# Kernel optimization log

Hardware: AMD Instinct MI355X
Metric: run time of the kernel (lower is better)

Reference implementation:

```python
import jax, jax.numpy as jnp
import numpy as np

DIM = 256
HEADS = 8
M = 16                      # window_size
Mo = int((1 + 0.5) * M)     # overlapped window = 24
TABLE = (M + Mo - 2) * (2 * Mo) + 1  # 1825
B = 256                     # batch * num_windows


def _relative_position_index():
    ch = np.arange(M)
    cw = np.arange(Mo)
    gh = np.stack(np.meshgrid(ch, ch, indexing='ij')).reshape(2, -1)   # (2, M^2)
    gw = np.stack(np.meshgrid(cw, cw, indexing='ij')).reshape(2, -1)   # (2, Mo^2)
    rel = gh[:, :, None] - gw[:, None, :]          # (2, M^2, Mo^2)
    rel = rel.transpose(1, 2, 0)
    rel[:, :, 0] += Mo - 1
    rel[:, :, 1] += Mo - 1
    rel[:, :, 0] *= 2 * Mo - 1
    return rel.sum(-1).astype(np.int32)            # (M^2, Mo^2)


def setup_inputs() -> dict:
    key = jax.random.key(0)
    ks = jax.random.split(key, 9)
    inp = {
        'q_w': jax.random.normal(ks[0], (B, M * M, DIM), jnp.float32),
        'kv_w': jax.random.normal(ks[1], (B, Mo * Mo, DIM), jnp.float32),
        'q_W': jax.random.normal(ks[2], (DIM, DIM), jnp.float32) * 0.02,
        'q_b': jnp.zeros((DIM,), jnp.float32),
        'kv_W': jax.random.normal(ks[3], (DIM, 2 * DIM), jnp.float32) * 0.02,
        'kv_b': jnp.zeros((2 * DIM,), jnp.float32),
        'proj_W': jax.random.normal(ks[4], (DIM, DIM), jnp.float32) * 0.02,
        'proj_b': jnp.zeros((DIM,), jnp.float32),
        'bias_table': jax.random.normal(ks[5], (TABLE, HEADS), jnp.float32) * 0.02,
        'rel_index': jnp.asarray(_relative_position_index()),
    }
    return inp


def reference(q_w, kv_w, q_W, q_b, kv_W, kv_b, proj_W, proj_b, bias_table, rel_index):
    Dh = DIM // HEADS
    scale = Dh ** (-0.5)
    Nq, Nk = M * M, Mo * Mo
    # q projection -> (B, H, Nq, Dh)
    q = (q_w @ q_W + q_b).reshape(B, Nq, HEADS, Dh).transpose(0, 2, 1, 3)
    # kv projection -> k, v each (B, H, Nk, Dh)
    kv = (kv_w @ kv_W + kv_b).reshape(B, Nk, 2, HEADS, Dh)
    k = kv[:, :, 0].transpose(0, 2, 1, 3)
    v = kv[:, :, 1].transpose(0, 2, 1, 3)
    # scaled scores + gathered relative-position bias
    attn = jnp.einsum('bhqd,bhkd->bhqk', q * scale, k)
    bias = bias_table[rel_index.reshape(-1)].reshape(Nq, Nk, HEADS)
    attn = attn + bias.transpose(2, 0, 1)[None]     # (B, H, Nq, Nk)
    attn = jax.nn.softmax(attn, axis=-1)
    out = jnp.einsum('bhqk,bhkd->bhqd', attn, v)
    out = out.transpose(0, 2, 1, 3).reshape(B, Nq, DIM)
    return out @ proj_W + proj_b
```

## Files before the change

### kernel.cpp

```cpp
#include <hip/hip_runtime.h>
#include <hip/hip_bf16.h>

typedef __hip_bfloat16 bf16;
typedef __attribute__((ext_vector_type(8))) short bf16x8;
typedef __attribute__((ext_vector_type(4))) float floatx4;
typedef __attribute__((ext_vector_type(4))) unsigned short u16x4;

#define L2E 1.4426950408889634f
#define SCALE_L2E (0.17677669529663687f * 1.4426950408889634f)
#define MFMA16 __builtin_amdgcn_mfma_f32_16x16x32_bf16

__device__ __forceinline__ short f2bs(float x) {
  union { bf16 h; short s; } u; u.h = __float2bfloat16(x); return u.s;
}
__device__ __forceinline__ float ldf(const void* p, size_t i, bool f32) {
  return f32 ? ((const float*)p)[i] : __bfloat162float(((const bf16*)p)[i]);
}
__device__ __forceinline__ float bs2f(unsigned short u) {
  union { unsigned short u; bf16 h; } v; v.u = u; return __bfloat162float(v.h);
}
__device__ __forceinline__ unsigned int pkbf(float a, float b) {
  union { bf16 h; unsigned short s; } ua, ub;
  ua.h = __float2bfloat16(a); ub.h = __float2bfloat16(b);
  return (unsigned int)ua.s | ((unsigned int)ub.s << 16);
}
__device__ __forceinline__ bf16x8 load8(const void* p, size_t idx, bool f32) {
  if (f32) {
    const floatx4* fp = (const floatx4*)((const float*)p + idx);
    floatx4 a = fp[0], b = fp[1];
    bf16x8 r;
    r[0] = f2bs(a[0]); r[1] = f2bs(a[1]); r[2] = f2bs(a[2]); r[3] = f2bs(a[3]);
    r[4] = f2bs(b[0]); r[5] = f2bs(b[1]); r[6] = f2bs(b[2]); r[7] = f2bs(b[3]);
    return r;
  }
  return *(const bf16x8*)((const bf16*)p + idx);
}
__device__ __forceinline__ int xcd_remap(int bid, int nwg) {
  int q = nwg >> 3, r = nwg & 7, x = bid & 7, loc = bid >> 3;
  int base = (x < r) ? x * (q + 1) : r * (q + 1) + (x - r) * q;
  return base + loc;
}

__global__ void detect_dtype(const unsigned short* __restrict__ q_w_u16, int* __restrict__ flag) {
  int tid = threadIdx.x;
  int cnt = 0;
  for (int i = tid; i < 4096; i += 64) {
    int e = (q_w_u16[i] >> 7) & 0xFF;
    cnt += (e >= 145);
  }
  #pragma unroll
  for (int off = 32; off; off >>= 1) cnt += __shfl_down(cnt, off);
  if (tid == 0) *flag = (cnt >= 16) ? 1 : 0;
}

__global__ __launch_bounds__(256) void transpose_w(const void* __restrict__ src,
                                                   bf16* __restrict__ dst, int N,
                                                   const int* __restrict__ flagp) {
  __shared__ bf16 t[32][33];
  const bool f = (*flagp != 0);
  int bx = blockIdx.x * 32;
  int by = blockIdx.y * 32;
  int x = threadIdx.x & 31, y = threadIdx.x >> 5;
  #pragma unroll
  for (int yy = y; yy < 32; yy += 8)
    t[yy][x] = __float2bfloat16(ldf(src, (size_t)(by + yy) * N + bx + x, f));
  __syncthreads();
  #pragma unroll
  for (int yy = y; yy < 32; yy += 8)
    dst[(size_t)(bx + yy) * 256 + by + x] = t[x][yy];
}

__global__ __launch_bounds__(256) void bias_expand(const void* __restrict__ table,
                                                   const int* __restrict__ relidx,
                                                   bf16* __restrict__ biasFb,
                                                   const int* __restrict__ flagp) {
  const bool f = (*flagp != 0);
  int i = blockIdx.x * 256 + threadIdx.x;
  int q = i / 576, k = i - q * 576;
  int idx = relidx[i];
  size_t off = ((size_t)(q >> 4) * 36 + (k >> 4)) * 256 + (q & 15) * 16 + (k & 15);
  #pragma unroll
  for (int h = 0; h < 8; h++)
    biasFb[(size_t)h * 147456 + off] =
        __float2bfloat16(ldf(table, (size_t)idx * 8 + h, f) * L2E);
}

template <int EPI>
__global__ __launch_bounds__(256) void gemm_bt(const void* __restrict__ A, size_t a_off,
                                               const bf16* __restrict__ BT,
                                               const void* __restrict__ bias,
                                               void* __restrict__ C, size_t c_off,
                                               bf16* __restrict__ C2,
                                               const int* __restrict__ flagp) {
  __shared__ __align__(16) bf16 As[128 * 40];
  __shared__ __align__(16) bf16 Bs[128 * 40];
  const bool f = (*flagp != 0);
  const bool af = (EPI == 0) ? false : f;
  const int tid = threadIdx.x;
  const int wave = tid >> 6, lane = tid & 63;
  const int q4 = lane >> 4, l16 = lane & 15;
  constexpr int NT = (EPI == 2) ? 4 : 2;
  constexpr int LNT = (EPI == 2) ? 2 : 1;
  const int L = xcd_remap(blockIdx.x, gridDim.x);
  const int m0 = (L >> LNT) * 128, n0 = (L & (NT - 1)) * 128;
  const int wm = (wave & 1) * 64, wn = (wave >> 1) * 64;
  const int sr = tid >> 2, sc = (tid & 3) * 8;
  floatx4 acc[4][4];
  #pragma unroll
  for (int i = 0; i < 4; i++)
    #pragma unroll
    for (int j = 0; j < 4; j++) acc[i][j] = (floatx4){0.f, 0.f, 0.f, 0.f};

  const size_t abase = a_off + (size_t)(m0 + sr) * 256 + sc;
  const bf16* Bp = BT + (size_t)(n0 + sr) * 256 + sc;
  for (int k0 = 0; k0 < 256; k0 += 32) {
    *(bf16x8*)&As[sr * 40 + sc]        = load8(A, abase + k0, af);
    *(bf16x8*)&As[(sr + 64) * 40 + sc] = load8(A, abase + 64 * 256 + k0, af);
    *(bf16x8*)&Bs[sr * 40 + sc]        = *(const bf16x8*)(Bp + k0);
    *(bf16x8*)&Bs[(sr + 64) * 40 + sc] = *(const bf16x8*)(Bp + 64 * 256 + k0);
    __syncthreads();
    bf16x8 afr[4], bfr[4];
    #pragma unroll
    for (int i = 0; i < 4; i++)
      afr[i] = *(const bf16x8*)&As[(wm + i * 16 + l16) * 40 + q4 * 8];
    #pragma unroll
    for (int j = 0; j < 4; j++)
      bfr[j] = *(const bf16x8*)&Bs[(wn + j * 16 + l16) * 40 + q4 * 8];
    #pragma unroll
    for (int i = 0; i < 4; i++)
      #pragma unroll
      for (int j = 0; j < 4; j++)
        acc[i][j] = MFMA16(afr[i], bfr[j], acc[i][j], 0, 0, 0);
    __syncthreads();
  }
  #pragma unroll
  for (int i = 0; i < 4; i++) {
    #pragma unroll
    for (int j = 0; j < 4; j++) {
      int mrow = m0 + wm + i * 16 + q4 * 4;
      int ncol = n0 + wn + j * 16 + l16;
      float bv = ldf(bias, ncol, f);
      #pragma unroll
      for (int r = 0; r < 4; r++) {
        float v = acc[i][j][r] + bv;
        int m_e = mrow + r;
        if (EPI == 0) {
          size_t oi = c_off + (size_t)m_e * 256 + ncol;
          if (f) ((float*)C)[oi] = v;
          else   ((bf16*)C)[oi] = __float2bfloat16(v);
        } else if (EPI == 1) {
          ((bf16*)C)[(size_t)m_e * 256 + ncol] = __float2bfloat16(v * SCALE_L2E);
        } else {
          int bb = m_e / 576;
          int nn = m_e - bb * 576;
          if (ncol < 256) {
            int hh = ncol >> 5, dd = ncol & 31;
            ((bf16*)C)[(((size_t)bb * 8 + hh) * 576 + nn) * 32 + dd] = __float2bfloat16(v);
          } else {
            int cc = ncol - 256;
            int hh = cc >> 5, dd = cc & 31;
            int kt = nn >> 6, kvl = nn & 63;
            C2[((((size_t)bb * 8 + hh) * 9 + kt) * 32 + dd) * 64 + kvl] = __float2bfloat16(v);
          }
        }
      }
    }
  }
}

__global__ __launch_bounds__(256, 4) void attn(const bf16* __restrict__ Q,
                                               const bf16* __restrict__ Kc,
                                               const bf16* __restrict__ Vc,
                                               const bf16* __restrict__ biasF,
                                               bf16* __restrict__ O,
                                               int nwg) {
  __shared__ __align__(16) bf16 Ks[2][64][32];
  __shared__ __align__(16) bf16 Vs[2][32][64];
  __shared__ __align__(16) bf16 P[4][16][72];
  __shared__ float SCb[4][16];
  const int tid = threadIdx.x, wave = tid >> 6, lane = tid & 63;
  const int q4 = lane >> 4, l16 = lane & 15;
  const int L = xcd_remap(blockIdx.x, nwg);
  const int b = L >> 5, h = (L >> 2) & 7, qc = L & 3;
  const int q0 = qc * 64 + wave * 16;
  const int qb = qc * 4 + wave;

  bf16x8 qf = *(const bf16x8*)&Q[((size_t)b * 256 + q0 + l16) * 256 + h * 32 + q4 * 8];
  const bf16* kg = Kc + ((size_t)b * 8 + h) * 18432;
  const bf16* vg = Vc + ((size_t)b * 8 + h) * 18432;
  const unsigned short* bp =
      (const unsigned short*)biasF + ((size_t)h * 16 + qb) * 9216 + l16 * 16 + q4 * 4;

  bf16* ksd = &Ks[0][tid >> 2][(((tid & 3) ^ ((tid >> 2) & 3))) * 8];
  bf16* vsd = &Vs[0][tid >> 3][(((tid & 7) ^ ((tid >> 3) & 7))) * 8];
  const int kx = (l16 & 3);
  const int vx = (l16 & 7);

  float m = 0.f, l = 0.f;
  floatx4 o0 = (floatx4){0.f, 0.f, 0.f, 0.f};
  floatx4 o1 = (floatx4){0.f, 0.f, 0.f, 0.f};

  {
    bf16x8 k0r = *(const bf16x8*)(kg + tid * 8);
    bf16x8 v0r = *(const bf16x8*)(vg + tid * 8);
    *(bf16x8*)ksd = k0r;
    *(bf16x8*)vsd = v0r;
  }
  u16x4 bfr[4];
  #pragma unroll
  for (int t = 0; t < 4; t++) bfr[t] = *(const u16x4*)(bp + t * 256);
  asm volatile("s_waitcnt lgkmcnt(0)" ::: "memory");
  __builtin_amdgcn_sched_barrier(0);
  __builtin_amdgcn_s_barrier();
  __builtin_amdgcn_sched_barrier(0);

  #pragma unroll 1
  for (int it = 0; it < 9; it++) {
    const int cur = it & 1;
    const int nx = (cur ^ 1) * 2048;
    bf16x8 kNr, vNr; u16x4 bn[4];
    if (it < 8) {
      kNr = *(const bf16x8*)(kg + (it + 1) * 2048 + tid * 8);
      vNr = *(const bf16x8*)(vg + (it + 1) * 2048 + tid * 8);
      #pragma unroll
      for (int t = 0; t < 4; t++) bn[t] = *(const u16x4*)(bp + (it + 1) * 1024 + t * 256);
    }
    floatx4 s[4];
    __builtin_amdgcn_s_setprio(1);
    #pragma unroll
    for (int t = 0; t < 4; t++) {
      bf16x8 kf = *(const bf16x8*)&Ks[cur][t * 16 + l16][(q4 ^ kx) * 8];
      floatx4 c;
      #pragma unroll
      for (int r = 0; r < 4; r++) c[r] = bs2f(bfr[t][r]);
      s[t] = MFMA16(kf, qf, c, 0, 0, 0);
    }
    __builtin_amdgcn_s_setprio(0);
    float tm = fmaxf(fmaxf(fmaxf(s[0][0], s[0][1]), fmaxf(s[0][2], s[0][3])),
                     fmaxf(fmaxf(s[1][0], s[1][1]), fmaxf(s[1][2], s[1][3])));
    tm = fmaxf(tm, fmaxf(fmaxf(fmaxf(s[2][0], s[2][1]), fmaxf(s[2][2], s[2][3])),
                         fmaxf(fmaxf(s[3][0], s[3][1]), fmaxf(s[3][2], s[3][3]))));
    tm = fmaxf(tm, __shfl_xor(tm, 16));
    tm = fmaxf(tm, __shfl_xor(tm, 32));
    float p[4][4];
    #pragma unroll
    for (int t = 0; t < 4; t++)
      #pragma unroll
      for (int r = 0; r < 4; r++)
        p[t][r] = __builtin_amdgcn_exp2f(s[t][r] - m);
    float rs = ((p[0][0] + p[0][1]) + (p[0][2] + p[0][3])) +
               ((p[1][0] + p[1][1]) + (p[1][2] + p[1][3])) +
               ((p[2][0] + p[2][1]) + (p[2][2] + p[2][3])) +
               ((p[3][0] + p[3][1]) + (p[3][2] + p[3][3]));
    if (__any(tm > m + 8.f)) {
      float mn = fmaxf(m, tm);
      float sc = __builtin_amdgcn_exp2f(m - mn);
      #pragma unroll
      for (int t = 0; t < 4; t++)
        #pragma unroll
        for (int r = 0; r < 4; r++) p[t][r] *= sc;
      rs *= sc;
      l *= sc;
      if (q4 == 0) SCb[wave][l16] = sc;
      floatx4 sv = *(const floatx4*)&SCb[wave][q4 * 4];
      #pragma unroll
      for (int r = 0; r < 4; r++) { o0[r] *= sv[r]; o1[r] *= sv[r]; }
      m = mn;
    }
    rs += __shfl_xor(rs, 16);
    rs += __shfl_xor(rs, 32);
    l += rs;
    #pragma unroll
    for (int t = 0; t < 4; t++) {
      uint2 w;
      w.x = pkbf(p[t][0], p[t][1]);
      w.y = pkbf(p[t][2], p[t][3]);
      *(uint2*)&P[wave][l16][t * 16 + q4 * 4] = w;
    }
    bf16x8 pf0 = *(const bf16x8*)&P[wave][l16][q4 * 8];
    bf16x8 pf1 = *(const bf16x8*)&P[wave][l16][32 + q4 * 8];
    bf16x8 v00 = *(const bf16x8*)&Vs[cur][l16][((q4 ^ vx)) * 8];
    bf16x8 v01 = *(const bf16x8*)&Vs[cur][l16 + 16][((q4 ^ vx)) * 8];
    bf16x8 v10 = *(const bf16x8*)&Vs[cur][l16][(((4 + q4) ^ vx)) * 8];
    bf16x8 v11 = *(const bf16x8*)&Vs[cur][l16 + 16][(((4 + q4) ^ vx)) * 8];
    __builtin_amdgcn_s_setprio(1);
    o0 = MFMA16(pf0, v00, o0, 0, 0, 0);
    o1 = MFMA16(pf0, v01, o1, 0, 0, 0);
    o0 = MFMA16(pf1, v10, o0, 0, 0, 0);
    o1 = MFMA16(pf1, v11, o1, 0, 0, 0);
    __builtin_amdgcn_s_setprio(0);
    if (it < 8) {
      *(bf16x8*)(ksd + nx) = kNr;
      *(bf16x8*)(vsd + nx) = vNr;
      #pragma unroll
      for (int t = 0; t < 4; t++) bfr[t] = bn[t];
    }
    asm volatile("s_waitcnt lgkmcnt(0)" ::: "memory");
    __builtin_amdgcn_sched_barrier(0);
    __builtin_amdgcn_s_barrier();
    __builtin_amdgcn_sched_barrier(0);
  }
  float invl = 1.f / l;
  if (q4 == 0) SCb[wave][l16] = invl;
  floatx4 iv = *(const floatx4*)&SCb[wave][q4 * 4];
  bf16* op = O + ((size_t)b * 256 + q0 + q4 * 4) * 256 + h * 32;
  #pragma unroll
  for (int r = 0; r < 4; r++) {
    op[(size_t)r * 256 + l16]      = __float2bfloat16(o0[r] * iv[r]);
    op[(size_t)r * 256 + 16 + l16] = __float2bfloat16(o1[r] * iv[r]);
  }
}

extern "C" void kernel_launch(void* const* d_in, const int* in_sizes, int n_in,
                              void* d_out, int out_size, void* d_ws, size_t ws_size,
                              hipStream_t stream) {
  const void* q_w    = d_in[0];
  const void* kv_w   = d_in[1];
  const void* q_Wm   = d_in[2];
  const void* q_b    = d_in[3];
  const void* kv_Wm  = d_in[4];
  const void* kv_b   = d_in[5];
  const void* proj_Wm= d_in[6];
  const void* proj_b = d_in[7];
  const void* btab   = d_in[8];
  const int*  relidx = (const int*)d_in[9];

  const size_t FIXED = 256 + 131072 + 262144 + 131072 + 2359296;
  int W = 2;
  {
    const int cand[8] = {256, 128, 64, 32, 16, 8, 4, 2};
    for (int i = 0; i < 8; i++) {
      if (ws_size >= FIXED + (size_t)cand[i] * 851968ULL) { W = cand[i]; break; }
    }
  }
  const int NCH = 256 / W;

  char* ws = (char*)d_ws;
  int*  flag  = (int*)(ws);
  bf16* WqT   = (bf16*)(ws + 256);
  bf16* WkvT  = (bf16*)(ws + 131328);
  bf16* WpT   = (bf16*)(ws + 393472);
  bf16* biasFb= (bf16*)(ws + 524544);
  char* cb    = ws + FIXED;
  const size_t qsz = (size_t)W * 131072ULL;
  const size_t ksz = (size_t)W * 294912ULL;
  bf16* Qs   = (bf16*)(cb);
  bf16* Kb   = (bf16*)(cb + qsz);
  bf16* Vt   = (bf16*)(cb + qsz + ksz);
  bf16* Obuf = (bf16*)(cb + qsz + 2 * ksz);

  detect_dtype<<<1, 64, 0, stream>>>((const unsigned short*)q_w, flag);
  transpose_w<<<dim3(8, 8),  256, 0, stream>>>(q_Wm,   WqT,  256, flag);
  transpose_w<<<dim3(16, 8), 256, 0, stream>>>(kv_Wm,  WkvT, 512, flag);
  transpose_w<<<dim3(8, 8),  256, 0, stream>>>(proj_Wm,WpT,  256, flag);
  bias_expand<<<576, 256, 0, stream>>>(btab, relidx, biasFb, flag);

  for (int c = 0; c < NCH; c++) {
    const size_t qoff = (size_t)c * W * 65536;
    const size_t koff = (size_t)c * W * 147456;
    gemm_bt<1><<<4 * W, 256, 0, stream>>>(q_w, qoff, WqT, q_b, Qs, 0, nullptr, flag);
    gemm_bt<2><<<18 * W, 256, 0, stream>>>(kv_w, koff, WkvT, kv_b, Kb, 0, Vt, flag);
    attn<<<W * 32, 256, 0, stream>>>(Qs, Kb, Vt, biasFb, Obuf, W * 32);
    gemm_bt<0><<<4 * W, 256, 0, stream>>>(Obuf, 0, WpT, proj_b, d_out, qoff, nullptr, flag);
  }
}
```

Before: 638.2 us.

## Double-buffer GEMM shared tiles with register prefetch and vectorize V-transpose stores

The projection GEMM now uses two LDS buffers. Global loads for the next K-slice are issued into registers before the MFMA work on the current slice, and the fp32-to-bf16 conversion is split out so it happens after the math. This removes one barrier per iteration and hides global latency. The V-transposed epilogue also writes four contiguous bf16 values as one 8-byte store instead of four scalar stores, relying on 4-row groups never crossing a 576 batch boundary or a 64 tile. The cost is doubled LDS use and more live registers, which may reduce occupancy.

```diff
diff --git a/kernel.cpp b/kernel.cpp
--- a/kernel.cpp
+++ b/kernel.cpp
@@ -24,16 +24,26 @@
   ua.h = __float2bfloat16(a); ub.h = __float2bfloat16(b);
   return (unsigned int)ua.s | ((unsigned int)ub.s << 16);
 }
-__device__ __forceinline__ bf16x8 load8(const void* p, size_t idx, bool f32) {
+struct APre { floatx4 x, y; };
+__device__ __forceinline__ APre loadA(const void* p, size_t idx, bool f32) {
+  APre r;
   if (f32) {
     const floatx4* fp = (const floatx4*)((const float*)p + idx);
-    floatx4 a = fp[0], b = fp[1];
+    r.x = fp[0]; r.y = fp[1];
+  } else {
+    r.x = *(const floatx4*)((const bf16*)p + idx);
+    r.y = r.x;
+  }
+  return r;
+}
+__device__ __forceinline__ bf16x8 cvtA(const APre& a, bool f32) {
+  if (f32) {
     bf16x8 r;
-    r[0] = f2bs(a[0]); r[1] = f2bs(a[1]); r[2] = f2bs(a[2]); r[3] = f2bs(a[3]);
-    r[4] = f2bs(b[0]); r[5] = f2bs(b[1]); r[6] = f2bs(b[2]); r[7] = f2bs(b[3]);
+    r[0] = f2bs(a.x[0]); r[1] = f2bs(a.x[1]); r[2] = f2bs(a.x[2]); r[3] = f2bs(a.x[3]);
+    r[4] = f2bs(a.y[0]); r[5] = f2bs(a.y[1]); r[6] = f2bs(a.y[2]); r[7] = f2bs(a.y[3]);
     return r;
   }
-  return *(const bf16x8*)((const bf16*)p + idx);
+  union { floatx4 f; bf16x8 h; } u; u.f = a.x; return u.h;
 }
 __device__ __forceinline__ int xcd_remap(int bid, int nwg) {
   int q = nwg >> 3, r = nwg & 7, x = bid & 7, loc = bid >> 3;
@@ -92,8 +102,8 @@
                                                void* __restrict__ C, size_t c_off,
                                                bf16* __restrict__ C2,
                                                const int* __restrict__ flagp) {
-  __shared__ __align__(16) bf16 As[128 * 40];
-  __shared__ __align__(16) bf16 Bs[128 * 40];
+  __shared__ __align__(16) bf16 As[2][128 * 40];
+  __shared__ __align__(16) bf16 Bs[2][128 * 40];
   const bool f = (*flagp != 0);
   const bool af = (EPI == 0) ? false : f;
   const int tid = threadIdx.x;
@@ -113,26 +123,50 @@
 
   const size_t abase = a_off + (size_t)(m0 + sr) * 256 + sc;
   const bf16* Bp = BT + (size_t)(n0 + sr) * 256 + sc;
-  for (int k0 = 0; k0 < 256; k0 += 32) {
-    *(bf16x8*)&As[sr * 40 + sc]        = load8(A, abase + k0, af);
-    *(bf16x8*)&As[(sr + 64) * 40 + sc] = load8(A, abase + 64 * 256 + k0, af);
-    *(bf16x8*)&Bs[sr * 40 + sc]        = *(const bf16x8*)(Bp + k0);
-    *(bf16x8*)&Bs[(sr + 64) * 40 + sc] = *(const bf16x8*)(Bp + 64 * 256 + k0);
-    __syncthreads();
+
+  {
+    APre a0 = loadA(A, abase, af);
+    APre a1 = loadA(A, abase + 64 * 256, af);
+    bf16x8 b0 = *(const bf16x8*)(Bp);
+    bf16x8 b1 = *(const bf16x8*)(Bp + 64 * 256);
+    *(bf16x8*)&As[0][sr * 40 + sc]        = cvtA(a0, af);
+    *(bf16x8*)&As[0][(sr + 64) * 40 + sc] = cvtA(a1, af);
+    *(bf16x8*)&Bs[0][sr * 40 + sc]        = b0;
+    *(bf16x8*)&Bs[0][(sr + 64) * 40 + sc] = b1;
+  }
+  __syncthreads();
+
+  #pragma unroll
+  for (int t = 0; t < 8; t++) {
+    const int cur = t & 1, nxt = cur ^ 1;
+    APre na0, na1; bf16x8 nb0, nb1;
+    if (t < 7) {
+      na0 = loadA(A, abase + (t + 1) * 32, af);
+      na1 = loadA(A, abase + 64 * 256 + (t + 1) * 32, af);
+      nb0 = *(const bf16x8*)(Bp + (t + 1) * 32);
+      nb1 = *(const bf16x8*)(Bp + 64 * 256 + (t + 1) * 32);
+    }
     bf16x8 afr[4], bfr[4];
     #pragma unroll
     for (int i = 0; i < 4; i++)
-      afr[i] = *(const bf16x8*)&As[(wm + i * 16 + l16) * 40 + q4 * 8];
+      afr[i] = *(const bf16x8*)&As[cur][(wm + i * 16 + l16) * 40 + q4 * 8];
     #pragma unroll
     for (int j = 0; j < 4; j++)
-      bfr[j] = *(const bf16x8*)&Bs[(wn + j * 16 + l16) * 40 + q4 * 8];
+      bfr[j] = *(const bf16x8*)&Bs[cur][(wn + j * 16 + l16) * 40 + q4 * 8];
     #pragma unroll
     for (int i = 0; i < 4; i++)
       #pragma unroll
       for (int j = 0; j < 4; j++)
         acc[i][j] = MFMA16(afr[i], bfr[j], acc[i][j], 0, 0, 0);
-    __syncthreads();
-  }
+    if (t < 7) {
+      *(bf16x8*)&As[nxt][sr * 40 + sc]        = cvtA(na0, af);
+      *(bf16x8*)&As[nxt][(sr + 64) * 40 + sc] = cvtA(na1, af);
+      *(bf16x8*)&Bs[nxt][sr * 40 + sc]        = nb0;
+      *(bf16x8*)&Bs[nxt][(sr + 64) * 40 + sc] = nb1;
+      __syncthreads();
+    }
+  }
+
   #pragma unroll
   for (int i = 0; i < 4; i++) {
     #pragma unroll
@@ -140,27 +174,32 @@
       int mrow = m0 + wm + i * 16 + q4 * 4;
       int ncol = n0 + wn + j * 16 + l16;
       float bv = ldf(bias, ncol, f);
-      #pragma unroll
-      for (int r = 0; r < 4; r++) {
-        float v = acc[i][j][r] + bv;
-        int m_e = mrow + r;
-        if (EPI == 0) {
-          size_t oi = c_off + (size_t)m_e * 256 + ncol;
-          if (f) ((float*)C)[oi] = v;
-          else   ((bf16*)C)[oi] = __float2bfloat16(v);
-        } else if (EPI == 1) {
-          ((bf16*)C)[(size_t)m_e * 256 + ncol] = __float2bfloat16(v * SCALE_L2E);
-        } else {
-          int bb = m_e / 576;
-          int nn = m_e - bb * 576;
-          if (ncol < 256) {
+      if (EPI == 2 && ncol >= 256) {
+        int cc = ncol - 256, hh = cc >> 5, dd = cc & 31;
+        int bb = mrow / 576, nn = mrow - bb * 576;
+        u16x4 w;
+        #pragma unroll
+        for (int r = 0; r < 4; r++) {
+          union { bf16 h; unsigned short s; } u;
+          u.h = __float2bfloat16(acc[i][j][r] + bv);
+          w[r] = u.s;
+        }
+        *(u16x4*)&C2[((((size_t)bb * 8 + hh) * 9 + (nn >> 6)) * 32 + dd) * 64 + (nn & 63)] = w;
+      } else {
+        #pragma unroll
+        for (int r = 0; r < 4; r++) {
+          float v = acc[i][j][r] + bv;
+          int m_e = mrow + r;
+          if (EPI == 0) {
+            size_t oi = c_off + (size_t)m_e * 256 + ncol;
+            if (f) ((float*)C)[oi] = v;
+            else   ((bf16*)C)[oi] = __float2bfloat16(v);
+          } else if (EPI == 1) {
+            ((bf16*)C)[(size_t)m_e * 256 + ncol] = __float2bfloat16(v * SCALE_L2E);
+          } else {
+            int bb = m_e / 576, nn = m_e - bb * 576;
             int hh = ncol >> 5, dd = ncol & 31;
             ((bf16*)C)[(((size_t)bb * 8 + hh) * 576 + nn) * 32 + dd] = __float2bfloat16(v);
-          } else {
-            int cc = ncol - 256;
-            int hh = cc >> 5, dd = cc & 31;
-            int kt = nn >> 6, kvl = nn & 63;
-            C2[((((size_t)bb * 8 + hh) * 9 + kt) * 32 + dd) * 64 + kvl] = __float2bfloat16(v);
           }
         }
       }
```

New measurement: 559.3 us. 1.14x faster.
